# Performance work log

Measured on AMD Instinct MI355X. Metric: run time of the kernel, lower is better.

The kernel has to match this reference:

```python
import jax, jax.numpy as jnp
import numpy as np

N, E, D, H, C = 100000, 1600000, 128, 128, 47
EPS = 1e-5


def setup_inputs() -> dict:
    key = jax.random.key(0)
    ks = jax.random.split(key, 10)
    s = 1.0 / np.sqrt(D).astype(np.float32)
    return {
        "x": jax.random.normal(ks[0], (N, D), jnp.float32),
        "edge_index": jax.random.randint(ks[1], (2, E), 0, N, jnp.int32),
        "Wl0": jax.random.normal(ks[2], (H, D), jnp.float32) * s,
        "bl0": jnp.zeros((H,), jnp.float32),
        "Wr0": jax.random.normal(ks[3], (H, D), jnp.float32) * s,
        "g0": jnp.ones((H,), jnp.float32),
        "b0": jnp.zeros((H,), jnp.float32),
        "Wl1": jax.random.normal(ks[4], (H, H), jnp.float32) * s,
        "bl1": jnp.zeros((H,), jnp.float32),
        "Wr1": jax.random.normal(ks[5], (H, H), jnp.float32) * s,
        "g1": jnp.ones((H,), jnp.float32),
        "b1": jnp.zeros((H,), jnp.float32),
        "Wl2": jax.random.normal(ks[6], (C, H), jnp.float32) * s,
        "bl2": jnp.zeros((C,), jnp.float32),
        "Wr2": jax.random.normal(ks[7], (C, H), jnp.float32) * s,
    }


def _sage_conv(x, edge_index, Wl, bl, Wr):
    # PyG SAGEConv(mean aggr): out = lin_l(mean_{j in N(i)} x_j) + lin_r(x_i)
    dst, src = edge_index[0], edge_index[1]
    n = x.shape[0]
    msg = x[src]                                             # [E, d] gather
    summed = jax.ops.segment_sum(msg, dst, num_segments=n)   # [N, d] scatter-add
    deg = jax.ops.segment_sum(jnp.ones((msg.shape[0],), x.dtype), dst, num_segments=n)
    agg = summed / jnp.maximum(deg, 1.0)[:, None]            # mean over neighbors
    return agg @ Wl.T + bl + x @ Wr.T


def _bn(x, g, b):
    # BatchNorm1d, training-mode batch statistics (biased variance)
    mu = jnp.mean(x, axis=0)
    var = jnp.mean(jnp.square(x - mu), axis=0)
    return (x - mu) * jax.lax.rsqrt(var + EPS) * g + b


def reference(x, edge_index, Wl0, bl0, Wr0, g0, b0, Wl1, bl1, Wr1, g1, b1, Wl2, bl2, Wr2):
    h = _sage_conv(x, edge_index, Wl0, bl0, Wr0)
    h = jax.nn.relu(_bn(h, g0, b0))          # dropout treated as identity (deterministic reference)
    h = _sage_conv(h, edge_index, Wl1, bl1, Wr1)
    h = jax.nn.relu(_bn(h, g1, b1))
    return _sage_conv(h, edge_index, Wl2, bl2, Wr2)
```

## Files before the change

kernel.cpp:

```cpp
#include <hip/hip_runtime.h>

typedef __attribute__((ext_vector_type(8))) short short8;
typedef __attribute__((ext_vector_type(4))) float f32x4;

constexpr float BN_EPS = 1e-5f;
#define NBUCKETS 128

__device__ __forceinline__ ushort f2bf(float f) {
  uint u = __float_as_uint(f);
  u = (u + 0x7fffu + ((u >> 16) & 1u)) >> 16;
  return (ushort)u;
}
__device__ __forceinline__ float bf2f(ushort h) { return __uint_as_float((uint)h << 16); }
__device__ __forceinline__ float bf2f_lo(uint v) { return __uint_as_float(v << 16); }
__device__ __forceinline__ float bf2f_hi(uint v) { return __uint_as_float(v & 0xffff0000u); }

typedef __attribute__((address_space(1))) const unsigned int* as1_cu32;
typedef __attribute__((address_space(3))) unsigned int* as3_u32;
__device__ __forceinline__ void gload_lds16(const void* g, void* l) {
  __builtin_amdgcn_global_load_lds((as1_cu32)g, (as3_u32)l, 16, 0, 0);
}


__global__ __launch_bounds__(256) void k_cast(const float* __restrict__ in, ushort* __restrict__ out, int n4) {
  for (int i = blockIdx.x * 256 + threadIdx.x; i < n4; i += gridDim.x * 256) {
    float4 v = reinterpret_cast<const float4*>(in)[i];
    ushort4 o;
    o.x = f2bf(v.x); o.y = f2bf(v.y); o.z = f2bf(v.z); o.w = f2bf(v.w);
    reinterpret_cast<ushort4*>(out)[i] = o;
  }
}

__global__ __launch_bounds__(256) void k_prep_weights(const float* __restrict__ Wl0, const float* __restrict__ Wr0,
                                                      const float* __restrict__ Wl1, const float* __restrict__ Wr1,
                                                      const float* __restrict__ Wl2, const float* __restrict__ Wr2,
                                                      ushort* __restrict__ W0l, ushort* __restrict__ W0r,
                                                      ushort* __restrict__ W1l, ushort* __restrict__ W1r,
                                                      ushort* __restrict__ Wc, int C) {
  int b = blockIdx.x;
  if (b < 64) {
    const float* src = (b < 16) ? Wl0 : (b < 32) ? Wr0 : (b < 48) ? Wl1 : Wr1;
    ushort* dst = (b < 16) ? W0l : (b < 32) ? W0r : (b < 48) ? W1l : W1r;
    int i = (b & 15) * 256 + threadIdx.x;
    float4 v = reinterpret_cast<const float4*>(src)[i];
    ushort4 o;
    o.x = f2bf(v.x); o.y = f2bf(v.y); o.z = f2bf(v.z); o.w = f2bf(v.w);
    reinterpret_cast<ushort4*>(dst)[i] = o;
  } else {
    int i = (b - 64) * 256 + threadIdx.x;
    int r = i >> 7, k = i & 127;
    float v = 0.f;
    if (r < C) v = Wl2[r * 128 + k];
    else if (r >= 64 && r < 64 + C) v = Wr2[(r - 64) * 128 + k];
    Wc[i] = f2bf(v);
  }
}


__global__ __launch_bounds__(256) void k_bucket_hist(const int* __restrict__ dst, int E, int* __restrict__ bcnt) {
  __shared__ int h[NBUCKETS];
  for (int i = threadIdx.x; i < NBUCKETS; i += 256) h[i] = 0;
  __syncthreads();
  for (int i = blockIdx.x * 256 + threadIdx.x; i < E; i += gridDim.x * 256)
    atomicAdd(&h[dst[i] >> 10], 1);
  __syncthreads();
  for (int i = threadIdx.x; i < NBUCKETS; i += 256)
    if (h[i]) atomicAdd(&bcnt[i], h[i]);
}

__global__ __launch_bounds__(128) void k_bucket_scan(const int* __restrict__ bcnt, int* __restrict__ brp,
                                                     int* __restrict__ bcur) {
  __shared__ int sh[NBUCKETS];
  int tid = threadIdx.x;
  int v = bcnt[tid];
  sh[tid] = v;
  __syncthreads();
  for (int off = 1; off < NBUCKETS; off <<= 1) {
    int t = (tid >= off) ? sh[tid - off] : 0;
    __syncthreads();
    sh[tid] += t;
    __syncthreads();
  }
  int ex = sh[tid] - v;
  brp[tid] = ex;
  bcur[tid] = ex;
  if (tid == NBUCKETS - 1) brp[NBUCKETS] = sh[tid];
}

__global__ __launch_bounds__(256) void k_binscatter(const int* __restrict__ dst, const int* __restrict__ src, int E,
                                                    int* __restrict__ bcur, uint* __restrict__ ebuf) {
  __shared__ int h[NBUCKETS];
  __shared__ int base[NBUCKETS];
  __shared__ int cur[NBUCKETS];
  const int e0 = blockIdx.x * 8192;
  const int e1 = min(e0 + 8192, E);
  for (int i = threadIdx.x; i < NBUCKETS; i += 256) h[i] = 0;
  __syncthreads();
  for (int e = e0 + threadIdx.x; e < e1; e += 256) atomicAdd(&h[dst[e] >> 10], 1);
  __syncthreads();
  if (threadIdx.x < NBUCKETS) {
    base[threadIdx.x] = atomicAdd(&bcur[threadIdx.x], h[threadIdx.x]);
    cur[threadIdx.x] = 0;
  }
  __syncthreads();
  for (int e = e0 + threadIdx.x; e < e1; e += 256) {
    int d = dst[e];
    int b = d >> 10;
    int pos = base[b] + atomicAdd(&cur[b], 1);
    ebuf[pos] = (uint)(d & 1023) | ((uint)src[e] << 10);
  }
}

__global__ __launch_bounds__(512) void k_bucket_build(const uint* __restrict__ ebuf, const int* __restrict__ brp,
                                                      int* __restrict__ rp, float* __restrict__ deg_inv,
                                                      int* __restrict__ csr, int N, int E) {
  __shared__ int cnt[1024];
  __shared__ int pre[1024];
  __shared__ int tmp[1024];
  const int blk = blockIdx.x, tid = threadIdx.x;
  const int base = blk << 10;
  const int p0 = brp[blk], p1 = brp[blk + 1];
  for (int i = tid; i < 1024; i += 512) cnt[i] = 0;
  __syncthreads();
  for (int p = p0 + tid; p < p1; p += 512) atomicAdd(&cnt[ebuf[p] & 1023u], 1);
  __syncthreads();
  for (int i = tid; i < 1024; i += 512) pre[i] = cnt[i];
  __syncthreads();
  for (int off = 1; off < 1024; off <<= 1) {
    for (int i = tid; i < 1024; i += 512) tmp[i] = (i >= off) ? pre[i - off] : 0;
    __syncthreads();
    for (int i = tid; i < 1024; i += 512) pre[i] += tmp[i];
    __syncthreads();
  }
  for (int i = tid; i < 1024; i += 512) {
    int node = base + i;
    if (node < N) {
      int ex = pre[i] - cnt[i];
      rp[node] = p0 + ex;
      deg_inv[node] = 1.0f / (float)max(cnt[i], 1);
    }
    tmp[i] = pre[i] - cnt[i];
  }
  if (tid == 0 && blk == gridDim.x - 1) rp[N] = E;
  __syncthreads();
  for (int p = p0 + tid; p < p1; p += 512) {
    uint pr = ebuf[p];
    int pos = p0 + atomicAdd(&tmp[pr & 1023u], 1);
    csr[pos] = (int)(pr >> 10);
  }
}


__global__ __launch_bounds__(256) void k_agg128(const ushort* __restrict__ X, const int* __restrict__ rp,
                                                const int* __restrict__ csr, const float* __restrict__ deg_inv,
                                                ushort* __restrict__ out, int N) {
  const int wave = threadIdx.x >> 6, lane = threadIdx.x & 63;
  const int sub = lane >> 4, li = lane & 15;
  const int node = blockIdx.x * 16 + wave * 4 + sub;
  if (node >= N) return;
  const int start = rp[node];
  const int c = rp[node + 1] - start;
  const uint4* X16 = reinterpret_cast<const uint4*>(X);
  float a0 = 0.f, a1 = 0.f, a2 = 0.f, a3 = 0.f, a4 = 0.f, a5 = 0.f, a6 = 0.f, a7 = 0.f;
  int p = 0;
  for (; p + 7 < c; p += 8) {
    int idx[8];
#pragma unroll
    for (int u = 0; u < 8; ++u) idx[u] = csr[start + p + u];
    uint4 v[8];
#pragma unroll
    for (int u = 0; u < 8; ++u) v[u] = X16[(size_t)idx[u] * 16 + li];
#pragma unroll
    for (int u = 0; u < 8; ++u) {
      a0 += bf2f_lo(v[u].x); a1 += bf2f_hi(v[u].x);
      a2 += bf2f_lo(v[u].y); a3 += bf2f_hi(v[u].y);
      a4 += bf2f_lo(v[u].z); a5 += bf2f_hi(v[u].z);
      a6 += bf2f_lo(v[u].w); a7 += bf2f_hi(v[u].w);
    }
  }
  if (p + 3 < c) {
    int idx[4];
#pragma unroll
    for (int u = 0; u < 4; ++u) idx[u] = csr[start + p + u];
    uint4 v[4];
#pragma unroll
    for (int u = 0; u < 4; ++u) v[u] = X16[(size_t)idx[u] * 16 + li];
#pragma unroll
    for (int u = 0; u < 4; ++u) {
      a0 += bf2f_lo(v[u].x); a1 += bf2f_hi(v[u].x);
      a2 += bf2f_lo(v[u].y); a3 += bf2f_hi(v[u].y);
      a4 += bf2f_lo(v[u].z); a5 += bf2f_hi(v[u].z);
      a6 += bf2f_lo(v[u].w); a7 += bf2f_hi(v[u].w);
    }
    p += 4;
  }
  for (; p < c; ++p) {
    uint4 v = X16[(size_t)csr[start + p] * 16 + li];
    a0 += bf2f_lo(v.x); a1 += bf2f_hi(v.x);
    a2 += bf2f_lo(v.y); a3 += bf2f_hi(v.y);
    a4 += bf2f_lo(v.z); a5 += bf2f_hi(v.z);
    a6 += bf2f_lo(v.w); a7 += bf2f_hi(v.w);
  }
  const float di = deg_inv[node];
  uint4 o;
  o.x = (uint)f2bf(a0 * di) | ((uint)f2bf(a1 * di) << 16);
  o.y = (uint)f2bf(a2 * di) | ((uint)f2bf(a3 * di) << 16);
  o.z = (uint)f2bf(a4 * di) | ((uint)f2bf(a5 * di) << 16);
  o.w = (uint)f2bf(a6 * di) | ((uint)f2bf(a7 * di) << 16);
  reinterpret_cast<uint4*>(out)[(size_t)node * 16 + li] = o;
}


template <bool DUAL>
__global__ __launch_bounds__(512, 6) void k_gemm(const ushort* __restrict__ A, const ushort* __restrict__ B,
                                                 const ushort* __restrict__ WA, const ushort* __restrict__ WB,
                                                 float* __restrict__ partial, ushort* __restrict__ Z, int M) {
  __shared__ ushort sA[64 * 128];
  __shared__ ushort sB[DUAL ? 64 * 128 : 64];
  __shared__ ushort sZ[64 * 128];
  const int tid = threadIdx.x;
  const int wave = tid >> 6, lane = tid & 63;
  const int rfrag = lane & 15, kgrp = lane >> 4;
  const int row0 = blockIdx.x * 64;

#pragma unroll
  for (int i = 0; i < 2; ++i) {
    int c = wave * 2 + i;
    int lb = c * 1024 + lane * 16;
    int row = lb >> 8, bin = lb & 255;
    int gr = min(row0 + row, M - 1);
    int sb = bin ^ ((row & 7) << 4);
    gload_lds16((const char*)A + (size_t)gr * 256 + sb, (char*)sA + c * 1024);
    if (DUAL) gload_lds16((const char*)B + (size_t)gr * 256 + sb, (char*)sB + c * 1024);
  }

  short8 wfA[4], wfB[4];
  {
    const ushort* wa = WA + (wave * 16 + rfrag) * 128 + kgrp * 8;
#pragma unroll
    for (int s = 0; s < 4; ++s) wfA[s] = *reinterpret_cast<const short8*>(wa + s * 32);
    if (DUAL) {
      const ushort* wb = WB + (wave * 16 + rfrag) * 128 + kgrp * 8;
#pragma unroll
      for (int s = 0; s < 4; ++s) wfB[s] = *reinterpret_cast<const short8*>(wb + s * 32);
    }
  }
  __syncthreads();

  f32x4 acc[4];
#pragma unroll
  for (int i = 0; i < 4; ++i) acc[i] = (f32x4){0.f, 0.f, 0.f, 0.f};

  const int rs = (rfrag & 7) << 4;
#pragma unroll
  for (int strip = 0; strip < 4; ++strip) {
    const int r = strip * 16 + rfrag;
    short8 af[4];
#pragma unroll
    for (int s = 0; s < 4; ++s)
      af[s] = *reinterpret_cast<const short8*>((const char*)sA + r * 256 + ((kgrp * 16 + s * 64) ^ rs));
#pragma unroll
    for (int s = 0; s < 4; ++s)
      acc[strip] = __builtin_amdgcn_mfma_f32_16x16x32_bf16(af[s], wfA[s], acc[strip], 0, 0, 0);
    if (DUAL) {
      short8 bf[4];
#pragma unroll
      for (int s = 0; s < 4; ++s)
        bf[s] = *reinterpret_cast<const short8*>((const char*)sB + r * 256 + ((kgrp * 16 + s * 64) ^ rs));
#pragma unroll
      for (int s = 0; s < 4; ++s)
        acc[strip] = __builtin_amdgcn_mfma_f32_16x16x32_bf16(bf[s], wfB[s], acc[strip], 0, 0, 0);
    }
  }

  if (DUAL) {
    float s1 = 0.f, s2 = 0.f;
#pragma unroll
    for (int strip = 0; strip < 4; ++strip) {
#pragma unroll
      for (int rr = 0; rr < 4; ++rr) {
        int grow = row0 + strip * 16 + kgrp * 4 + rr;
        if (grow < M) {
          float v = acc[strip][rr];
          s1 += v;
          s2 = fmaf(v, v, s2);
        }
      }
    }
    s1 += __shfl_xor(s1, 16); s2 += __shfl_xor(s2, 16);
    s1 += __shfl_xor(s1, 32); s2 += __shfl_xor(s2, 32);
    if (kgrp == 0) {
      partial[(size_t)blockIdx.x * 256 + wave * 16 + rfrag] = s1;
      partial[(size_t)blockIdx.x * 256 + 128 + wave * 16 + rfrag] = s2;
    }
  }

  const int cb = (wave * 16 + rfrag) * 2;
#pragma unroll
  for (int strip = 0; strip < 4; ++strip) {
#pragma unroll
    for (int rr = 0; rr < 4; ++rr) {
      int row = strip * 16 + kgrp * 4 + rr;
      *reinterpret_cast<ushort*>((char*)sZ + row * 256 + (cb ^ ((row & 7) << 4))) = f2bf(acc[strip][rr]);
    }
  }
  __syncthreads();

#pragma unroll
  for (int i = 0; i < 2; ++i) {
    int lb = (wave * 2 + i) * 1024 + lane * 16;
    int row = lb >> 8, bin = lb & 255;
    int gr = row0 + row;
    if (gr < M)
      *reinterpret_cast<uint4*>((char*)Z + (size_t)gr * 256 + bin) =
          *reinterpret_cast<const uint4*>((const char*)sZ + row * 256 + (bin ^ ((row & 7) << 4)));
  }
}


__global__ __launch_bounds__(256) void k_bn_reduce(const float* __restrict__ partial, int nblk,
                                                   float* __restrict__ stats) {
  float acc = 0.f;
  for (int b = blockIdx.x; b < nblk; b += gridDim.x) acc += partial[(size_t)b * 256 + threadIdx.x];
  atomicAdd(&stats[threadIdx.x], acc);
}

__global__ __launch_bounds__(128) void k_bn_finalize(const float* __restrict__ sums, const float* __restrict__ g,
                                                     const float* __restrict__ b, int M, float* __restrict__ ss) {
  int f = threadIdx.x;
  float inv = 1.0f / (float)M;
  float mean = sums[f] * inv;
  float var = sums[128 + f] * inv - mean * mean;
  var = fmaxf(var, 0.f);
  float sc = g[f] * rsqrtf(var + BN_EPS);
  ss[f] = sc;
  ss[128 + f] = fmaf(-mean, sc, b[f]);
}

__global__ __launch_bounds__(256) void k_bn_relu(uint2* __restrict__ Z, int n2, const float* __restrict__ ss) {
  for (int i = blockIdx.x * 256 + threadIdx.x; i < n2; i += gridDim.x * 256) {
    uint2 v = Z[i];
    int f0 = (i & 31) * 4;
    float4 sc = *reinterpret_cast<const float4*>(&ss[f0]);
    float4 sh = *reinterpret_cast<const float4*>(&ss[128 + f0]);
    float a0 = fmaxf(fmaf(bf2f_lo(v.x), sc.x, sh.x), 0.f);
    float a1 = fmaxf(fmaf(bf2f_hi(v.x), sc.y, sh.y), 0.f);
    float a2 = fmaxf(fmaf(bf2f_lo(v.y), sc.z, sh.z), 0.f);
    float a3 = fmaxf(fmaf(bf2f_hi(v.y), sc.w, sh.w), 0.f);
    v.x = (uint)f2bf(a0) | ((uint)f2bf(a1) << 16);
    v.y = (uint)f2bf(a2) | ((uint)f2bf(a3) << 16);
    Z[i] = v;
  }
}


__global__ __launch_bounds__(256) void k_agg47(const ushort* __restrict__ Z, const float* __restrict__ bias,
                                               const int* __restrict__ rp, const int* __restrict__ csr,
                                               const float* __restrict__ deg_inv, float* __restrict__ out,
                                               int N, int C) {
  const int wave = threadIdx.x >> 6, lane = threadIdx.x & 63;
  const int sub = lane >> 3, li = lane & 7;
  const int node = blockIdx.x * 32 + wave * 8 + sub;
  if (node >= N) return;
  const int start = rp[node];
  const int c = rp[node + 1] - start;
  const uint4* Z16 = reinterpret_cast<const uint4*>(Z);
  float a0 = 0.f, a1 = 0.f, a2 = 0.f, a3 = 0.f, a4 = 0.f, a5 = 0.f, a6 = 0.f, a7 = 0.f;
  int p = 0;
  for (; p + 7 < c; p += 8) {
    int idx[8];
#pragma unroll
    for (int u = 0; u < 8; ++u) idx[u] = csr[start + p + u];
    uint4 v[8];
#pragma unroll
    for (int u = 0; u < 8; ++u) v[u] = Z16[(size_t)idx[u] * 16 + li];
#pragma unroll
    for (int u = 0; u < 8; ++u) {
      a0 += bf2f_lo(v[u].x); a1 += bf2f_hi(v[u].x);
      a2 += bf2f_lo(v[u].y); a3 += bf2f_hi(v[u].y);
      a4 += bf2f_lo(v[u].z); a5 += bf2f_hi(v[u].z);
      a6 += bf2f_lo(v[u].w); a7 += bf2f_hi(v[u].w);
    }
  }
  for (; p < c; ++p) {
    uint4 v = Z16[(size_t)csr[start + p] * 16 + li];
    a0 += bf2f_lo(v.x); a1 += bf2f_hi(v.x);
    a2 += bf2f_lo(v.y); a3 += bf2f_hi(v.y);
    a4 += bf2f_lo(v.z); a5 += bf2f_hi(v.z);
    a6 += bf2f_lo(v.w); a7 += bf2f_hi(v.w);
  }
  const float di = deg_inv[node];
  uint4 sv = Z16[(size_t)node * 16 + 8 + li];
  float s[8] = {bf2f_lo(sv.x), bf2f_hi(sv.x), bf2f_lo(sv.y), bf2f_hi(sv.y),
                bf2f_lo(sv.z), bf2f_hi(sv.z), bf2f_lo(sv.w), bf2f_hi(sv.w)};
  float a[8] = {a0, a1, a2, a3, a4, a5, a6, a7};
#pragma unroll
  for (int j = 0; j < 8; ++j) {
    int f = li * 8 + j;
    if (f < C) out[(size_t)node * C + f] = fmaf(a[j], di, s[j] + bias[f]);
  }
}


extern "C" void kernel_launch(void* const* d_in, const int* in_sizes, int n_in,
                              void* d_out, int out_size, void* d_ws, size_t ws_size,
                              hipStream_t stream) {
  const float* x   = (const float*)d_in[0];
  const int*   ei  = (const int*)d_in[1];
  const float* Wl0 = (const float*)d_in[2];
  const float* Wr0 = (const float*)d_in[4];
  const float* g0  = (const float*)d_in[5];
  const float* b0  = (const float*)d_in[6];
  const float* Wl1 = (const float*)d_in[7];
  const float* Wr1 = (const float*)d_in[9];
  const float* g1  = (const float*)d_in[10];
  const float* b1  = (const float*)d_in[11];
  const float* Wl2 = (const float*)d_in[12];
  const float* bl2 = (const float*)d_in[13];
  const float* Wr2 = (const float*)d_in[14];

  const int N = in_sizes[0] / 128;
  const int E = in_sizes[1] / 2;
  const int C = in_sizes[13];

  const int* edst = ei;
  const int* esrc = ei + E;

  char* w = (char*)d_ws;
  auto al = [](size_t v) { return (v + 255) & ~(size_t)255; };
  size_t off = 0;
  int*    bcnt    = (int*)(w + off);    off = al(off + NBUCKETS * 4);
  int*    brp     = (int*)(w + off);    off = al(off + (NBUCKETS + 1) * 4);
  int*    bcur    = (int*)(w + off);    off = al(off + NBUCKETS * 4);
  float*  stats   = (float*)(w + off);  off = al(off + 512 * 4);
  int*    rp      = (int*)(w + off);    off = al(off + (size_t)(N + 1) * 4);
  float*  deg_inv = (float*)(w + off);  off = al(off + (size_t)N * 4);
  int*    csr     = (int*)(w + off);    off = al(off + (size_t)E * 4);
  uint*   ebuf    = (uint*)(w + off);   off = al(off + (size_t)E * 4);
  ushort* Xb      = (ushort*)(w + off); off = al(off + (size_t)N * 128 * 2);
  ushort* hA      = (ushort*)(w + off); off = al(off + (size_t)N * 128 * 2);
  ushort* hB      = (ushort*)(w + off); off = al(off + (size_t)N * 128 * 2);
  ushort* W0l     = (ushort*)(w + off); off = al(off + 16384 * 2);
  ushort* W0r     = (ushort*)(w + off); off = al(off + 16384 * 2);
  ushort* W1l     = (ushort*)(w + off); off = al(off + 16384 * 2);
  ushort* W1r     = (ushort*)(w + off); off = al(off + 16384 * 2);
  ushort* Wc      = (ushort*)(w + off); off = al(off + 16384 * 2);
  const int nblkG = (N + 63) / 64;
  float*  partial = (float*)(w + off);  off = al(off + (size_t)nblkG * 256 * 4);

  const int nbBuck = (N + 1023) / 1024;
  const int binGrid = (E + 8191) / 8192;
  const int agg128Grid = (N + 15) / 16;
  const int agg47Grid = (N + 31) / 32;

  k_cast<<<2048, 256, 0, stream>>>(x, Xb, N * 32);
  k_prep_weights<<<128, 256, 0, stream>>>(Wl0, Wr0, Wl1, Wr1, Wl2, Wr2, W0l, W0r, W1l, W1r, Wc, C);

  hipMemsetAsync(bcnt, 0, NBUCKETS * 4, stream);
  k_bucket_hist<<<256, 256, 0, stream>>>(edst, E, bcnt);
  k_bucket_scan<<<1, 128, 0, stream>>>(bcnt, brp, bcur);
  k_binscatter<<<binGrid, 256, 0, stream>>>(edst, esrc, E, bcur, ebuf);
  k_bucket_build<<<nbBuck, 512, 0, stream>>>(ebuf, brp, rp, deg_inv, csr, N, E);

  k_agg128<<<agg128Grid, 256, 0, stream>>>(Xb, rp, csr, deg_inv, hA, N);
  k_gemm<true><<<nblkG, 512, 0, stream>>>(hA, Xb, W0l, W0r, partial, hB, N);
  hipMemsetAsync(stats, 0, 256 * 4, stream);
  k_bn_reduce<<<64, 256, 0, stream>>>(partial, nblkG, stats);
  k_bn_finalize<<<1, 128, 0, stream>>>(stats, g0, b0, N, stats + 256);
  k_bn_relu<<<2048, 256, 0, stream>>>((uint2*)hB, N * 32, stats + 256);

  k_agg128<<<agg128Grid, 256, 0, stream>>>(hB, rp, csr, deg_inv, hA, N);
  k_gemm<true><<<nblkG, 512, 0, stream>>>(hA, hB, W1l, W1r, partial, hB, N);
  hipMemsetAsync(stats, 0, 256 * 4, stream);
  k_bn_reduce<<<64, 256, 0, stream>>>(partial, nblkG, stats);
  k_bn_finalize<<<1, 128, 0, stream>>>(stats, g1, b1, N, stats + 256);
  k_bn_relu<<<2048, 256, 0, stream>>>((uint2*)hB, N * 32, stats + 256);

  k_gemm<false><<<nblkG, 512, 0, stream>>>(hB, nullptr, Wc, nullptr, nullptr, hA, N);
  k_agg47<<<agg47Grid, 256, 0, stream>>>(hA, bl2, rp, csr, deg_inv, (float*)d_out, N, C);
}
```

Before: 348.8 us.

## Sort nodes by degree for aggregation and split final GEMM output into compact halves

Adds a degree histogram and a counting-sort permutation so that the aggregation kernels process nodes grouped by in-degree, which reduces divergence among lanes that share a wave. The final GEMM now writes its neighbor half and its self half into separate compact arrays with a 128-byte stride, so the last aggregation gathers denser rows. The cost is two extra small kernels plus a memset, and output writes and node lookups now follow a permuted order, which loses locality across neighboring node ids.

```diff
diff --git a/kernel.cpp b/kernel.cpp
--- a/kernel.cpp
+++ b/kernel.cpp
@@ -113,14 +113,17 @@
 
 __global__ __launch_bounds__(512) void k_bucket_build(const uint* __restrict__ ebuf, const int* __restrict__ brp,
                                                       int* __restrict__ rp, float* __restrict__ deg_inv,
-                                                      int* __restrict__ csr, int N, int E) {
+                                                      int* __restrict__ csr, int* __restrict__ dhist,
+                                                      int N, int E) {
   __shared__ int cnt[1024];
   __shared__ int pre[1024];
   __shared__ int tmp[1024];
+  __shared__ int dh[64];
   const int blk = blockIdx.x, tid = threadIdx.x;
   const int base = blk << 10;
   const int p0 = brp[blk], p1 = brp[blk + 1];
   for (int i = tid; i < 1024; i += 512) cnt[i] = 0;
+  if (tid < 64) dh[tid] = 0;
   __syncthreads();
   for (int p = p0 + tid; p < p1; p += 512) atomicAdd(&cnt[ebuf[p] & 1023u], 1);
   __syncthreads();
@@ -138,6 +141,7 @@
       int ex = pre[i] - cnt[i];
       rp[node] = p0 + ex;
       deg_inv[node] = 1.0f / (float)max(cnt[i], 1);
+      atomicAdd(&dh[min(cnt[i], 63)], 1);
     }
     tmp[i] = pre[i] - cnt[i];
   }
@@ -148,16 +152,56 @@
     int pos = p0 + atomicAdd(&tmp[pr & 1023u], 1);
     csr[pos] = (int)(pr >> 10);
   }
+  if (tid < 64 && dh[tid]) atomicAdd(&dhist[tid], dh[tid]);
+}
+
+
+__global__ __launch_bounds__(64) void k_deg_scan(const int* __restrict__ dhist, int* __restrict__ dcur) {
+  __shared__ int sh[64];
+  int t = threadIdx.x;
+  int v = dhist[t];
+  sh[t] = v;
+  __syncthreads();
+  for (int off = 1; off < 64; off <<= 1) {
+    int u = (t >= off) ? sh[t - off] : 0;
+    __syncthreads();
+    sh[t] += u;
+    __syncthreads();
+  }
+  dcur[t] = sh[t] - v;
+}
+
+__global__ __launch_bounds__(512) void k_deg_scatter(const int* __restrict__ rp, int N,
+                                                     int* __restrict__ dcur, int* __restrict__ perm) {
+  __shared__ int h[64], base[64], cur[64];
+  const int n0 = blockIdx.x * 8192;
+  const int n1 = min(n0 + 8192, N);
+  if (threadIdx.x < 64) h[threadIdx.x] = 0;
+  __syncthreads();
+  for (int i = n0 + threadIdx.x; i < n1; i += 512)
+    atomicAdd(&h[min(rp[i + 1] - rp[i], 63)], 1);
+  __syncthreads();
+  if (threadIdx.x < 64) {
+    base[threadIdx.x] = atomicAdd(&dcur[threadIdx.x], h[threadIdx.x]);
+    cur[threadIdx.x] = 0;
+  }
+  __syncthreads();
+  for (int i = n0 + threadIdx.x; i < n1; i += 512) {
+    int d = min(rp[i + 1] - rp[i], 63);
+    perm[base[d] + atomicAdd(&cur[d], 1)] = i;
+  }
 }
 
 
 __global__ __launch_bounds__(256) void k_agg128(const ushort* __restrict__ X, const int* __restrict__ rp,
                                                 const int* __restrict__ csr, const float* __restrict__ deg_inv,
+                                                const int* __restrict__ perm,
                                                 ushort* __restrict__ out, int N) {
   const int wave = threadIdx.x >> 6, lane = threadIdx.x & 63;
   const int sub = lane >> 4, li = lane & 15;
-  const int node = blockIdx.x * 16 + wave * 4 + sub;
-  if (node >= N) return;
+  const int gi = blockIdx.x * 16 + wave * 4 + sub;
+  if (gi >= N) return;
+  const int node = perm[gi];
   const int start = rp[node];
   const int c = rp[node + 1] - start;
   const uint4* X16 = reinterpret_cast<const uint4*>(X);
@@ -214,7 +258,8 @@
 template <bool DUAL>
 __global__ __launch_bounds__(512, 6) void k_gemm(const ushort* __restrict__ A, const ushort* __restrict__ B,
                                                  const ushort* __restrict__ WA, const ushort* __restrict__ WB,
-                                                 float* __restrict__ partial, ushort* __restrict__ Z, int M) {
+                                                 float* __restrict__ partial, ushort* __restrict__ Z,
+                                                 ushort* __restrict__ Z2, int M) {
   __shared__ ushort sA[64 * 128];
   __shared__ ushort sB[DUAL ? 64 * 128 : 64];
   __shared__ ushort sZ[64 * 128];
@@ -311,9 +356,15 @@
     int lb = (wave * 2 + i) * 1024 + lane * 16;
     int row = lb >> 8, bin = lb & 255;
     int gr = row0 + row;
-    if (gr < M)
-      *reinterpret_cast<uint4*>((char*)Z + (size_t)gr * 256 + bin) =
-          *reinterpret_cast<const uint4*>((const char*)sZ + row * 256 + (bin ^ ((row & 7) << 4)));
+    if (gr < M) {
+      uint4 v = *reinterpret_cast<const uint4*>((const char*)sZ + row * 256 + (bin ^ ((row & 7) << 4)));
+      if (DUAL) {
+        *reinterpret_cast<uint4*>((char*)Z + (size_t)gr * 256 + bin) = v;
+      } else {
+        if (bin < 128) *reinterpret_cast<uint4*>((char*)Z + (size_t)gr * 128 + bin) = v;
+        else *reinterpret_cast<uint4*>((char*)Z2 + (size_t)gr * 128 + (bin - 128)) = v;
+      }
+    }
   }
 }
 
@@ -354,17 +405,19 @@
 }
 
 
-__global__ __launch_bounds__(256) void k_agg47(const ushort* __restrict__ Z, const float* __restrict__ bias,
-                                               const int* __restrict__ rp, const int* __restrict__ csr,
-                                               const float* __restrict__ deg_inv, float* __restrict__ out,
+__global__ __launch_bounds__(256) void k_agg47(const ushort* __restrict__ Yb, const ushort* __restrict__ Rb,
+                                               const float* __restrict__ bias, const int* __restrict__ rp,
+                                               const int* __restrict__ csr, const float* __restrict__ deg_inv,
+                                               const int* __restrict__ perm, float* __restrict__ out,
                                                int N, int C) {
   const int wave = threadIdx.x >> 6, lane = threadIdx.x & 63;
   const int sub = lane >> 3, li = lane & 7;
-  const int node = blockIdx.x * 32 + wave * 8 + sub;
-  if (node >= N) return;
+  const int gi = blockIdx.x * 32 + wave * 8 + sub;
+  if (gi >= N) return;
+  const int node = perm[gi];
   const int start = rp[node];
   const int c = rp[node + 1] - start;
-  const uint4* Z16 = reinterpret_cast<const uint4*>(Z);
+  const uint4* Y16 = reinterpret_cast<const uint4*>(Yb);
   float a0 = 0.f, a1 = 0.f, a2 = 0.f, a3 = 0.f, a4 = 0.f, a5 = 0.f, a6 = 0.f, a7 = 0.f;
   int p = 0;
   for (; p + 7 < c; p += 8) {
@@ -373,7 +426,7 @@
     for (int u = 0; u < 8; ++u) idx[u] = csr[start + p + u];
     uint4 v[8];
 #pragma unroll
-    for (int u = 0; u < 8; ++u) v[u] = Z16[(size_t)idx[u] * 16 + li];
+    for (int u = 0; u < 8; ++u) v[u] = Y16[(size_t)idx[u] * 8 + li];
 #pragma unroll
     for (int u = 0; u < 8; ++u) {
       a0 += bf2f_lo(v[u].x); a1 += bf2f_hi(v[u].x);
@@ -383,14 +436,14 @@
     }
   }
   for (; p < c; ++p) {
-    uint4 v = Z16[(size_t)csr[start + p] * 16 + li];
+    uint4 v = Y16[(size_t)csr[start + p] * 8 + li];
     a0 += bf2f_lo(v.x); a1 += bf2f_hi(v.x);
     a2 += bf2f_lo(v.y); a3 += bf2f_hi(v.y);
     a4 += bf2f_lo(v.z); a5 += bf2f_hi(v.z);
     a6 += bf2f_lo(v.w); a7 += bf2f_hi(v.w);
   }
   const float di = deg_inv[node];
-  uint4 sv = Z16[(size_t)node * 16 + 8 + li];
+  uint4 sv = reinterpret_cast<const uint4*>(Rb)[(size_t)node * 8 + li];
   float s[8] = {bf2f_lo(sv.x), bf2f_hi(sv.x), bf2f_lo(sv.y), bf2f_hi(sv.y),
                 bf2f_lo(sv.z), bf2f_hi(sv.z), bf2f_lo(sv.w), bf2f_hi(sv.w)};
   float a[8] = {a0, a1, a2, a3, a4, a5, a6, a7};
@@ -432,9 +485,12 @@
   int*    bcnt    = (int*)(w + off);    off = al(off + NBUCKETS * 4);
   int*    brp     = (int*)(w + off);    off = al(off + (NBUCKETS + 1) * 4);
   int*    bcur    = (int*)(w + off);    off = al(off + NBUCKETS * 4);
+  int*    dhist   = (int*)(w + off);    off = al(off + 64 * 4);
+  int*    dcur    = (int*)(w + off);    off = al(off + 64 * 4);
   float*  stats   = (float*)(w + off);  off = al(off + 512 * 4);
   int*    rp      = (int*)(w + off);    off = al(off + (size_t)(N + 1) * 4);
   float*  deg_inv = (float*)(w + off);  off = al(off + (size_t)N * 4);
+  int*    perm    = (int*)(w + off);    off = al(off + (size_t)N * 4);
   int*    csr     = (int*)(w + off);    off = al(off + (size_t)E * 4);
   uint*   ebuf    = (uint*)(w + off);   off = al(off + (size_t)E * 4);
   ushort* Xb      = (ushort*)(w + off); off = al(off + (size_t)N * 128 * 2);
@@ -448,8 +504,12 @@
   const int nblkG = (N + 63) / 64;
   float*  partial = (float*)(w + off);  off = al(off + (size_t)nblkG * 256 * 4);
 
+  ushort* Yb = hA;
+  ushort* Rb = hA + (size_t)N * 64;
+
   const int nbBuck = (N + 1023) / 1024;
   const int binGrid = (E + 8191) / 8192;
+  const int degGrid = (N + 8191) / 8192;
   const int agg128Grid = (N + 15) / 16;
   const int agg47Grid = (N + 31) / 32;
 
@@ -457,25 +517,28 @@
   k_prep_weights<<<128, 256, 0, stream>>>(Wl0, Wr0, Wl1, Wr1, Wl2, Wr2, W0l, W0r, W1l, W1r, Wc, C);
 
   hipMemsetAsync(bcnt, 0, NBUCKETS * 4, stream);
+  hipMemsetAsync(dhist, 0, 64 * 4, stream);
   k_bucket_hist<<<256, 256, 0, stream>>>(edst, E, bcnt);
   k_bucket_scan<<<1, 128, 0, stream>>>(bcnt, brp, bcur);
   k_binscatter<<<binGrid, 256, 0, stream>>>(edst, esrc, E, bcur, ebuf);
-  k_bucket_build<<<nbBuck, 512, 0, stream>>>(ebuf, brp, rp, deg_inv, csr, N, E);
-
-  k_agg128<<<agg128Grid, 256, 0, stream>>>(Xb, rp, csr, deg_inv, hA, N);
-  k_gemm<true><<<nblkG, 512, 0, stream>>>(hA, Xb, W0l, W0r, partial, hB, N);
+  k_bucket_build<<<nbBuck, 512, 0, stream>>>(ebuf, brp, rp, deg_inv, csr, dhist, N, E);
+  k_deg_scan<<<1, 64, 0, stream>>>(dhist, dcur);
+  k_deg_scatter<<<degGrid, 512, 0, stream>>>(rp, N, dcur, perm);
+
+  k_agg128<<<agg128Grid, 256, 0, stream>>>(Xb, rp, csr, deg_inv, perm, hA, N);
+  k_gemm<true><<<nblkG, 512, 0, stream>>>(hA, Xb, W0l, W0r, partial, hB, nullptr, N);
   hipMemsetAsync(stats, 0, 256 * 4, stream);
   k_bn_reduce<<<64, 256, 0, stream>>>(partial, nblkG, stats);
   k_bn_finalize<<<1, 128, 0, stream>>>(stats, g0, b0, N, stats + 256);
   k_bn_relu<<<2048, 256, 0, stream>>>((uint2*)hB, N * 32, stats + 256);
 
-  k_agg128<<<agg128Grid, 256, 0, stream>>>(hB, rp, csr, deg_inv, hA, N);
-  k_gemm<true><<<nblkG, 512, 0, stream>>>(hA, hB, W1l, W1r, partial, hB, N);
+  k_agg128<<<agg128Grid, 256, 0, stream>>>(hB, rp, csr, deg_inv, perm, hA, N);
+  k_gemm<true><<<nblkG, 512, 0, stream>>>(hA, hB, W1l, W1r, partial, hB, nullptr, N);
   hipMemsetAsync(stats, 0, 256 * 4, stream);
   k_bn_reduce<<<64, 256, 0, stream>>>(partial, nblkG, stats);
   k_bn_finalize<<<1, 128, 0, stream>>>(stats, g1, b1, N, stats + 256);
   k_bn_relu<<<2048, 256, 0, stream>>>((uint2*)hB, N * 32, stats + 256);
 
-  k_gemm<false><<<nblkG, 512, 0, stream>>>(hB, nullptr, Wc, nullptr, nullptr, hA, N);
-  k_agg47<<<agg47Grid, 256, 0, stream>>>(hA, bl2, rp, csr, deg_inv, (float*)d_out, N, C);
-}
+  k_gemm<false><<<nblkG, 512, 0, stream>>>(hB, nullptr, Wc, nullptr, nullptr, Yb, Rb, N);
+  k_agg47<<<agg47Grid, 256, 0, stream>>>(Yb, Rb, bl2, rp, csr, deg_inv, perm, (float*)d_out, N, C);
+}
```

New measurement: 360.7 us. +3.4%, slower.
